# Performance work log

Hardware: AMD Instinct MI355X
Metric: run time of the kernel (lower is better)

## Reference

```python
import jax, jax.numpy as jnp
import numpy as np

H = 4  # fixed number of heads in the layer


def setup_inputs() -> dict:
    key = jax.random.key(0)
    ks = jax.random.split(key, 6)
    B, S, D = 4, 2048, 512
    U = 2 * D  # per-head projection width (units = d_model * 2)
    x = jax.random.normal(ks[0], (B, S, D), dtype=jnp.float32)
    gamma = jnp.ones((D,), dtype=jnp.float32)
    beta = jnp.zeros((D,), dtype=jnp.float32)
    s = 0.02
    Wq = jax.random.normal(ks[1], (H, D, U), dtype=jnp.float32) * s
    Wk = jax.random.normal(ks[2], (H, D, U), dtype=jnp.float32) * s
    Wv = jax.random.normal(ks[3], (H, D, U), dtype=jnp.float32) * s
    Wout = jax.random.normal(ks[4], (H * U, D), dtype=jnp.float32) * s
    return {"x": x, "gamma": gamma, "beta": beta, "Wq": Wq, "Wk": Wk, "Wv": Wv, "Wout": Wout}


def _forward(x, gamma, beta, Wq, Wk, Wv, Wout):
    B, S, D = x.shape
    eps = 1e-6
    # LayerNormalization over last axis (Keras default, eps=1e-6)
    mu = jnp.mean(x, axis=-1, keepdims=True)
    var = jnp.mean(jnp.square(x - mu), axis=-1, keepdims=True)
    xn = (x - mu) * jax.lax.rsqrt(var + eps) * gamma + beta
    # Per-head Q/K/V projections, batched over head axis. Dropout is identity at inference.
    q = jnp.einsum('bsd,hdu->bhsu', xn, Wq)
    k = jnp.einsum('bsd,hdu->bhsu', xn, Wk)
    v = jnp.einsum('bsd,hdu->bhsu', xn, Wv)
    # Keras Attention(use_scale=False, causal=True): unscaled dot-product scores
    scores = jnp.einsum('bhsu,bhtu->bhst', q, k)  # [B,H,S,S]
    causal = jnp.tril(jnp.ones((S, S), dtype=bool))
    scores = jnp.where(causal, scores, jnp.finfo(scores.dtype).min)
    probs = jax.nn.softmax(scores, axis=-1)
    head = jnp.einsum('bhst,bhtu->bhsu', probs, v)  # [B,H,S,U]
    # concat heads in head order -> [B,S,H*U], then output Dense back to D
    HU = head.shape[1] * head.shape[3]
    cat = head.transpose(0, 2, 1, 3).reshape(B, S, HU)
    return cat @ Wout


def reference(x, gamma, beta, Wq, Wk, Wv, Wout):
    return _forward(x, gamma, beta, Wq, Wk, Wv, Wout)
```

## Files before the change

kernel.cpp:

```cpp
#include <hip/hip_runtime.h>

typedef _Float16 half8 __attribute__((ext_vector_type(8)));
typedef float floatx4 __attribute__((ext_vector_type(4)));

__device__ __forceinline__ void gl16(const _Float16* g, _Float16* l) {
    __builtin_amdgcn_global_load_lds((const __attribute__((address_space(1))) void*)g,
                                     (__attribute__((address_space(3))) void*)l, 16, 0, 0);
}

__device__ __forceinline__ half8 dsr16(const _Float16* p) {
    half8 r;
    const __attribute__((address_space(3))) _Float16* lp =
        (const __attribute__((address_space(3))) _Float16*)p;
    asm volatile("ds_read_b128 %0, %1" : "=v"(r) : "v"(lp));
    return r;
}

#define Scst 2048
#define Dcst 512
#define Ucst 1024
#define Hcst 4
#define SDo 1048576LL
#define UDo 524288LL
#define SUo 2097152LL
#define SSo 4194304LL
#define USo 2097152LL
#define SHUo 8388608LL

__global__ __launch_bounds__(64) void ln_k(const float* __restrict__ x,
                                           const float* __restrict__ gamma,
                                           const float* __restrict__ beta,
                                           _Float16* __restrict__ xn) {
    const int D = 512;
    long long base = (long long)blockIdx.x * D;
    int lane = threadIdx.x;
    floatx4 x0 = *(const floatx4*)(x + base + lane * 8);
    floatx4 x1 = *(const floatx4*)(x + base + lane * 8 + 4);
    float f[8];
#pragma unroll
    for (int i = 0; i < 4; i++) { f[i] = x0[i]; f[4 + i] = x1[i]; }
    float s = 0.f, ss = 0.f;
#pragma unroll
    for (int i = 0; i < 8; i++) { s += f[i]; ss += f[i] * f[i]; }
#pragma unroll
    for (int off = 32; off; off >>= 1) { s += __shfl_xor(s, off); ss += __shfl_xor(ss, off); }
    float mean = s * (1.f / 512.f);
    float var = ss * (1.f / 512.f) - mean * mean;
    float rstd = rsqrtf(var + 1e-6f);
    floatx4 g0 = *(const floatx4*)(gamma + lane * 8);
    floatx4 g1 = *(const floatx4*)(gamma + lane * 8 + 4);
    floatx4 b0 = *(const floatx4*)(beta + lane * 8);
    floatx4 b1 = *(const floatx4*)(beta + lane * 8 + 4);
    half8 o;
#pragma unroll
    for (int i = 0; i < 4; i++) {
        o[i]     = (_Float16)((f[i]     - mean) * rstd * g0[i] + b0[i]);
        o[4 + i] = (_Float16)((f[4 + i] - mean) * rstd * g1[i] + b1[i]);
    }
    *(half8*)(xn + base + lane * 8) = o;
}

__global__ __launch_bounds__(256) void tr_k(const float* __restrict__ in,
                                            _Float16* __restrict__ out, int R, int C) {
    __shared__ _Float16 tile[32][33];
    int tx = threadIdx.x, ty = threadIdx.y;
    long long zo = (long long)blockIdx.z * R * C;
    int r0 = blockIdx.y * 32, c0 = blockIdx.x * 32;
    for (int yy = ty; yy < 32; yy += 8)
        tile[yy][tx] = (_Float16)in[zo + (long long)(r0 + yy) * C + c0 + tx];
    __syncthreads();
    for (int yy = ty; yy < 32; yy += 8)
        out[zo + (long long)(c0 + yy) * R + r0 + tx] = tile[tx][yy];
}

#define BM 128
#define BN 128
#define BK 32
__global__ __launch_bounds__(256) void gemm_bt(
    const _Float16* __restrict__ A, const _Float16* __restrict__ Bt, void* __restrict__ Cv,
    int K, int ldc, int cflags, int mode) {
    int z = blockIdx.z;
    long long offA = 0, offB = 0, offC = 0;
    switch (mode) {
        case 1:
            offA = (long long)((z >> 2) & 1) * SDo;
            offB = (long long)(((z >> 3) * 4) + (z & 3)) * UDo;
            offC = (long long)(((z >> 3) * 8) + ((z & 3) * 2) + ((z >> 2) & 1)) * SUo;
            break;
        case 2:
            offA = (long long)z * SUo; offB = (long long)z * SUo; offC = (long long)z * SSo;
            break;
        case 3:
            offA = (long long)(z >> 1) * UDo; offB = (long long)(z & 1) * SDo;
            offC = (long long)z * USo;
            break;
        case 4:
            offA = (long long)z * SSo; offB = (long long)z * USo;
            offC = (long long)(z & 1) * SHUo + (long long)(z >> 1) * Ucst;
            break;
        case 6:
            offB = (long long)(z & 7) * UDo; offC = (long long)z * SUo;
            break;
        case 7:
            offA = (long long)(z & 3) * UDo; offC = (long long)z * USo;
            break;
        default: break;
    }
    const _Float16* Ab = A + offA;
    const _Float16* Bb = Bt + offB;

    int gx = gridDim.x, gy = gridDim.y;
    int nb = gx * gy;
    int lin = blockIdx.y * gx + blockIdx.x;
    int mIdx, nIdx;
    if (((nb & 7) == 0) && ((gx & 3) == 0)) {
        int chunk = nb >> 3;
        int vid = (lin >> 3) + chunk * (lin & 7);
        int panelH = gy * 4;
        int panel = vid / panelH;
        int rem = vid - panel * panelH;
        mIdx = rem >> 2;
        nIdx = (panel << 2) + (rem & 3);
    } else { mIdx = blockIdx.y; nIdx = blockIdx.x; }
    int m0 = mIdx * BM, n0 = nIdx * BN;

    if ((cflags & 4) && n0 > m0 + (BM - 1)) return;
    int kend = (cflags & 8) ? min(K, m0 + BM) : K;

    __shared__ _Float16 As[2][BM * BK];
    __shared__ _Float16 Bs[2][BN * BK];

    int t = threadIdx.x;
    int srow = t >> 2;
    int scol = (t & 3) * 8;
    int lane = t & 63, w = t >> 6;
    int wm = (w >> 1) * 64, wn = (w & 1) * 64;
    int lm = lane & 15, lk = (lane >> 4) * 8;

    floatx4 acc[4][4];
#pragma unroll
    for (int i = 0; i < 4; i++)
#pragma unroll
        for (int j = 0; j < 4; j++) acc[i][j] = floatx4{0.f, 0.f, 0.f, 0.f};

    const _Float16* ga0 = Ab + (long long)(m0 + srow) * K + scol;
    const _Float16* ga1 = Ab + (long long)(m0 + 64 + srow) * K + scol;
    const _Float16* gb0 = Bb + (long long)(n0 + srow) * K + scol;
    const _Float16* gb1 = Bb + (long long)(n0 + 64 + srow) * K + scol;

    int nIter = kend / BK;
    gl16(ga0, &As[0][t * 8]);
    gl16(ga1, &As[0][2048 + t * 8]);
    gl16(gb0, &Bs[0][t * 8]);
    gl16(gb1, &Bs[0][2048 + t * 8]);

    for (int it = 0; it < nIter; it++) {
        __syncthreads();
        int cur = it & 1;
        half8 af[4], bfr[4];
#pragma unroll
        for (int i = 0; i < 4; i++) af[i] = *(const half8*)&As[cur][(wm + i * 16 + lm) * BK + lk];
#pragma unroll
        for (int j = 0; j < 4; j++) bfr[j] = *(const half8*)&Bs[cur][(wn + j * 16 + lm) * BK + lk];
        if (it + 1 < nIter) {
            int nk = (it + 1) * BK;
            int nxt = cur ^ 1;
            gl16(ga0 + nk, &As[nxt][t * 8]);
            gl16(ga1 + nk, &As[nxt][2048 + t * 8]);
            gl16(gb0 + nk, &Bs[nxt][t * 8]);
            gl16(gb1 + nk, &Bs[nxt][2048 + t * 8]);
        }
#pragma unroll
        for (int i = 0; i < 4; i++)
#pragma unroll
            for (int j = 0; j < 4; j++)
                acc[i][j] = __builtin_amdgcn_mfma_f32_16x16x32_f16(af[i], bfr[j], acc[i][j], 0, 0, 0);
    }

    int cr = (lane >> 4) * 4;
    int cc = lm;
    bool outf32 = (cflags & 1) != 0;
#pragma unroll
    for (int i = 0; i < 4; i++) {
#pragma unroll
        for (int j = 0; j < 4; j++) {
            int rr = m0 + wm + i * 16 + cr;
            int nn = n0 + wn + j * 16 + cc;
#pragma unroll
            for (int r2 = 0; r2 < 4; r2++) {
                long long idx = (long long)(rr + r2) * ldc + nn + offC;
                float val = acc[i][j][r2];
                if (outf32) ((float*)Cv)[idx] = val;
                else ((_Float16*)Cv)[idx] = (_Float16)val;
            }
        }
    }
}

__global__ __launch_bounds__(512, 2) void gemm_bt256(
    const _Float16* __restrict__ A, const _Float16* __restrict__ Bt, void* __restrict__ Cv,
    int K, int ldc, int cflags, int mode) {
    int z = blockIdx.z;
    long long offA = 0, offB = 0, offC = 0;
    switch (mode) {
        case 1:
            offA = (long long)((z >> 2) & 1) * SDo;
            offB = (long long)(((z >> 3) * 4) + (z & 3)) * UDo;
            offC = (long long)(((z >> 3) * 8) + ((z & 3) * 2) + ((z >> 2) & 1)) * SUo;
            break;
        case 2:
            offA = (long long)z * SUo; offB = (long long)z * SUo; offC = (long long)z * SSo;
            break;
        case 3:
            offA = (long long)(z >> 1) * UDo; offB = (long long)(z & 1) * SDo;
            offC = (long long)z * USo;
            break;
        case 4:
            offA = (long long)z * SSo; offB = (long long)z * USo;
            offC = (long long)(z & 1) * SHUo + (long long)(z >> 1) * Ucst;
            break;
        default: break;
    }
    const _Float16* Ab = A + offA;
    const _Float16* Bb = Bt + offB;

    int gx = gridDim.x;
    int nwg = gx * gridDim.y;
    int lin = blockIdx.y * gx + blockIdx.x;
    int q8 = nwg >> 3, r8 = nwg & 7;
    int xcd = lin & 7, sub8 = lin >> 3;
    int wg = (xcd < r8 ? xcd * (q8 + 1) : r8 * (q8 + 1) + (xcd - r8) * q8) + sub8;
    int m0 = (wg / gx) * 256, n0 = (wg % gx) * 256;

    if ((cflags & 4) && n0 > m0 + 255) return;
    int kend = (cflags & 8) ? min(K, m0 + 256) : K;
    int NT = kend >> 6;

    __shared__ _Float16 As2[2][2][8192];
    __shared__ _Float16 Bs2[2][2][8192];

    int t = threadIdx.x;
    int lane = t & 63, w = t >> 6;
    int wm = (w >> 2) * 128, wn = (w & 3) * 64;
    int lm = lane & 15, ls = lane >> 4;
    int sw8 = ((ls ^ ((lm >> 1) & 3)) << 3);

    long long stoff = (long long)(t >> 2) * K + (((t & 3) ^ ((t >> 3) & 3)) << 3);
    const _Float16* gA = Ab + (long long)m0 * K + stoff;
    const _Float16* gB = Bb + (long long)n0 * K + stoff;
    long long rowK = 128LL * K;
    int ldd = t * 8;

    floatx4 acc[8][4];
#pragma unroll
    for (int i = 0; i < 8; i++)
#pragma unroll
        for (int j = 0; j < 4; j++) acc[i][j] = floatx4{0.f, 0.f, 0.f, 0.f};

#define STGA(v, ks) { const _Float16* s_ = gA + (((v) << 6) + ((ks) << 5)); \
        gl16(s_, &As2[(v) & 1][ks][ldd]); gl16(s_ + rowK, &As2[(v) & 1][ks][4096 + ldd]); }
#define STGB(v, ks) { const _Float16* s_ = gB + (((v) << 6) + ((ks) << 5)); \
        gl16(s_, &Bs2[(v) & 1][ks][ldd]); gl16(s_ + rowK, &Bs2[(v) & 1][ks][4096 + ldd]); }
#define RDA(mm, ks) dsr16(&As2[cur][ks][(wm + (mm) * 16 + lm) * 32 + sw8])
#define RDB(nn, ks) dsr16(&Bs2[cur][ks][(wn + (nn) * 16 + lm) * 32 + sw8])
#define MFMA16(mh) \
    _Pragma("unroll") for (int mm = 0; mm < 4; mm++) \
    _Pragma("unroll") for (int nn = 0; nn < 4; nn++) \
        acc[(mh) * 4 + mm][nn] = __builtin_amdgcn_mfma_f32_16x16x32_f16( \
            af[mm], bf[nn], acc[(mh) * 4 + mm][nn], 0, 0, 0);

    STGA(0, 0) STGB(0, 0) STGA(0, 1) STGB(0, 1)
    if (NT > 1) { STGA(1, 0) STGB(1, 0) }
    if (NT > 1) asm volatile("s_waitcnt vmcnt(8)" ::: "memory");
    else        asm volatile("s_waitcnt vmcnt(4)" ::: "memory");
    __builtin_amdgcn_s_barrier();

    for (int tt = 0; tt < NT; tt++) {
        int cur = tt & 1;
        half8 af[4], bf[4];
        bf[0] = RDB(0, 0); bf[1] = RDB(1, 0); bf[2] = RDB(2, 0); bf[3] = RDB(3, 0);
        af[0] = RDA(0, 0); af[1] = RDA(1, 0); af[2] = RDA(2, 0); af[3] = RDA(3, 0);
        if (tt + 1 < NT) STGA(tt + 1, 1)
        __builtin_amdgcn_s_barrier();
        asm volatile("s_waitcnt lgkmcnt(0)" ::: "memory");
        __builtin_amdgcn_sched_barrier(0);
        __builtin_amdgcn_s_setprio(1);
        MFMA16(0)
        __builtin_amdgcn_s_setprio(0);
        __builtin_amdgcn_s_barrier();
        af[0] = RDA(4, 0); af[1] = RDA(5, 0); af[2] = RDA(6, 0); af[3] = RDA(7, 0);
        if (tt + 1 < NT) STGB(tt + 1, 1)
        if (tt + 1 < NT) asm volatile("s_waitcnt vmcnt(8)" ::: "memory");
        else             asm volatile("s_waitcnt vmcnt(0)" ::: "memory");
        __builtin_amdgcn_s_barrier();
        asm volatile("s_waitcnt lgkmcnt(0)" ::: "memory");
        __builtin_amdgcn_sched_barrier(0);
        __builtin_amdgcn_s_setprio(1);
        MFMA16(1)
        __builtin_amdgcn_s_setprio(0);
        __builtin_amdgcn_s_barrier();
        bf[0] = RDB(0, 1); bf[1] = RDB(1, 1); bf[2] = RDB(2, 1); bf[3] = RDB(3, 1);
        af[0] = RDA(0, 1); af[1] = RDA(1, 1); af[2] = RDA(2, 1); af[3] = RDA(3, 1);
        if (tt + 2 < NT) STGA(tt + 2, 0)
        __builtin_amdgcn_s_barrier();
        asm volatile("s_waitcnt lgkmcnt(0)" ::: "memory");
        __builtin_amdgcn_sched_barrier(0);
        __builtin_amdgcn_s_setprio(1);
        MFMA16(0)
        __builtin_amdgcn_s_setprio(0);
        __builtin_amdgcn_s_barrier();
        af[0] = RDA(4, 1); af[1] = RDA(5, 1); af[2] = RDA(6, 1); af[3] = RDA(7, 1);
        if (tt + 2 < NT) STGB(tt + 2, 0)
        if (tt + 2 < NT)      asm volatile("s_waitcnt vmcnt(8)" ::: "memory");
        else if (tt + 1 < NT) asm volatile("s_waitcnt vmcnt(4)" ::: "memory");
        else                  asm volatile("s_waitcnt vmcnt(0)" ::: "memory");
        __builtin_amdgcn_s_barrier();
        asm volatile("s_waitcnt lgkmcnt(0)" ::: "memory");
        __builtin_amdgcn_sched_barrier(0);
        __builtin_amdgcn_s_setprio(1);
        MFMA16(1)
        __builtin_amdgcn_s_setprio(0);
        __builtin_amdgcn_s_barrier();
    }

    int cr = ls * 4, cc = lm;
    bool outf32 = (cflags & 1) != 0;
#pragma unroll
    for (int i = 0; i < 8; i++) {
#pragma unroll
        for (int j = 0; j < 4; j++) {
            int rr = m0 + wm + i * 16 + cr;
            int nn = n0 + wn + j * 16 + cc;
#pragma unroll
            for (int r2 = 0; r2 < 4; r2++) {
                long long idx = (long long)(rr + r2) * ldc + nn + offC;
                float val = acc[i][j][r2];
                if (outf32) ((float*)Cv)[idx] = val;
                else ((_Float16*)Cv)[idx] = (_Float16)val;
            }
        }
    }
#undef STGA
#undef STGB
#undef RDA
#undef RDB
#undef MFMA16
}

__global__ __launch_bounds__(256) void softmax_h(_Float16* __restrict__ sc, int S) {
    int wid = threadIdx.x >> 6, lane = threadIdx.x & 63;
    int idx = blockIdx.x * 4 + wid;
    int r = idx & (S - 1);
    _Float16* srow = sc + (long long)idx * S;
    int nc = r >> 9;
    float v[32];
    float mx = -3.0e38f;
    for (int c = 0; c <= nc; c++) {
        half8 hv = *(half8*)(srow + lane * 8 + c * 512);
#pragma unroll
        for (int i = 0; i < 8; i++) {
            int n = lane * 8 + c * 512 + i;
            float s = (n <= r) ? (float)hv[i] : -3.0e38f;
            v[c * 8 + i] = s; mx = fmaxf(mx, s);
        }
    }
#pragma unroll
    for (int off = 32; off; off >>= 1) mx = fmaxf(mx, __shfl_xor(mx, off));
    float sum = 0.f;
    for (int c = 0; c <= nc; c++)
#pragma unroll
        for (int i = 0; i < 8; i++) {
            int n = lane * 8 + c * 512 + i;
            float e = (n <= r) ? __expf(v[c * 8 + i] - mx) : 0.f;
            v[c * 8 + i] = e; sum += e;
        }
#pragma unroll
    for (int off = 32; off; off >>= 1) sum += __shfl_xor(sum, off);
    float inv = 1.f / sum;
    for (int c = 0; c <= nc; c++) {
        half8 o;
#pragma unroll
        for (int i = 0; i < 8; i++) o[i] = (_Float16)(v[c * 8 + i] * inv);
        *(half8*)(srow + lane * 8 + c * 512) = o;
    }
}

extern "C" void kernel_launch(void* const* d_in, const int* in_sizes, int n_in,
                              void* d_out, int out_size, void* d_ws, size_t ws_size,
                              hipStream_t stream) {
    const int B = 4, S = 2048, D = 512, H = 4, U = 1024;
    const float* x     = (const float*)d_in[0];
    const float* gamma = (const float*)d_in[1];
    const float* beta  = (const float*)d_in[2];
    const float* Wq    = (const float*)d_in[3];
    const float* Wk    = (const float*)d_in[4];
    const float* Wv    = (const float*)d_in[5];
    const float* Wout  = (const float*)d_in[6];
    float* out = (float*)d_out;

    char* ws = (char*)d_ws;
    const size_t MiB = 1ull << 20;
    const long long SD = SDo, UD = UDo, SU = SUo, US = USo;

    _Float16* xn  = (_Float16*)(ws + 0);
    _Float16* WqT = (_Float16*)(ws + 8  * MiB);
    _Float16* WkT = (_Float16*)(ws + 12 * MiB);
    _Float16* WvT = (_Float16*)(ws + 16 * MiB);
    _Float16* WoT = (_Float16*)(ws + 20 * MiB);

    tr_k<<<dim3(U / 32, D / 32, H), dim3(32, 8), 0, stream>>>(Wq, WqT, D, U);
    tr_k<<<dim3(U / 32, D / 32, H), dim3(32, 8), 0, stream>>>(Wk, WkT, D, U);
    tr_k<<<dim3(U / 32, D / 32, H), dim3(32, 8), 0, stream>>>(Wv, WvT, D, U);
    tr_k<<<dim3(D / 32, (H * U) / 32, 1), dim3(32, 8), 0, stream>>>(Wout, WoT, H * U, D);
    ln_k<<<B * S, 64, 0, stream>>>(x, gamma, beta, xn);

    if (ws_size >= 168 * MiB) {
        _Float16* qk  = (_Float16*)(ws + 24 * MiB);
        _Float16* kk  = qk + 8 * SU;
        _Float16* sc  = (_Float16*)(ws + 88 * MiB);
        _Float16* vt  = qk;
        _Float16* cat = kk;

        for (int p = 0; p < 2; p++) {
            const _Float16* xnp = xn + (long long)p * 2 * SD;
            float* outp = out + (long long)p * 2 * SD;
            gemm_bt256<<<dim3(U / 256, S / 256, 16), 512, 0, stream>>>(xnp, WqT, qk, D, U, 0, 1);
            gemm_bt256<<<dim3(S / 256, S / 256, 8), 512, 0, stream>>>(qk, kk, sc, U, S, 4, 2);
            softmax_h<<<8 * S / 4, 256, 0, stream>>>(sc, S);
            gemm_bt256<<<dim3(S / 256, U / 256, 8), 512, 0, stream>>>(WvT, xnp, vt, D, S, 0, 3);
            gemm_bt256<<<dim3(U / 256, S / 256, 8), 512, 0, stream>>>(sc, vt, cat, S, H * U, 8, 4);
            gemm_bt<<<dim3(D / 128, 2 * S / 128, 1), 256, 0, stream>>>(cat, WoT, outp,
                H * U, D, 1, 0);
        }
    } else {
        _Float16* qb   = (_Float16*)(ws + 24 * MiB);
        _Float16* vTb  = (_Float16*)(ws + 56 * MiB);
        _Float16* catb = (_Float16*)(ws + 72 * MiB);
        _Float16* sc   = (_Float16*)(ws + 88 * MiB);

        for (int b = 0; b < B; b++) {
            const _Float16* xnb = xn + (long long)b * SD;
            gemm_bt<<<dim3(U / 128, S / 128, 2 * H), 256, 0, stream>>>(xnb, WqT, qb, D, U, 0, 6);
            gemm_bt<<<dim3(S / 128, U / 128, H), 256, 0, stream>>>(WvT, xnb, vTb, D, S, 0, 7);
            for (int h = 0; h < H; h++) {
                gemm_bt<<<dim3(S / 128, S / 128, 1), 256, 0, stream>>>(qb + (long long)h * SU,
                    qb + (long long)(H + h) * SU, sc, U, S, 4, 0);
                softmax_h<<<S / 4, 256, 0, stream>>>(sc, S);
                gemm_bt<<<dim3(U / 128, S / 128, 1), 256, 0, stream>>>(sc,
                    vTb + (long long)h * US, (void*)(catb + (long long)h * U), S, H * U, 8, 0);
            }
            gemm_bt<<<dim3(D / 128, S / 128, 1), 256, 0, stream>>>(catb, WoT,
                (void*)(out + (long long)b * SD), H * U, D, 1, 0);
        }
    }
}
```

Before: 663.5 us.

## Restructure GEMM main loop to two barriers per K-step with staggered LDS waits

The GEMM main loop is rebuilt so each K-substep loads all eight A fragments and four B fragments at once, with one barrier per substep instead of four. Partial lgkmcnt waits let the first half of the MFMAs start while the remaining LDS reads are still in flight. The global-to-LDS prefetches for A and B are now issued together after each MFMA block. This removes barrier stalls but raises register pressure (eight A fragments live). It also drops the NT==1 guard in the prologue, which assumes at least two K tiles.

```diff
diff --git a/kernel.cpp b/kernel.cpp
--- a/kernel.cpp
+++ b/kernel.cpp
@@ -263,64 +263,50 @@
         gl16(s_, &Bs2[(v) & 1][ks][ldd]); gl16(s_ + rowK, &Bs2[(v) & 1][ks][4096 + ldd]); }
 #define RDA(mm, ks) dsr16(&As2[cur][ks][(wm + (mm) * 16 + lm) * 32 + sw8])
 #define RDB(nn, ks) dsr16(&Bs2[cur][ks][(wn + (nn) * 16 + lm) * 32 + sw8])
-#define MFMA16(mh) \
-    _Pragma("unroll") for (int mm = 0; mm < 4; mm++) \
+#define MFMAH(m0_, m1_) \
+    _Pragma("unroll") for (int mm = (m0_); mm < (m1_); mm++) \
     _Pragma("unroll") for (int nn = 0; nn < 4; nn++) \
-        acc[(mh) * 4 + mm][nn] = __builtin_amdgcn_mfma_f32_16x16x32_f16( \
-            af[mm], bf[nn], acc[(mh) * 4 + mm][nn], 0, 0, 0);
-
-    STGA(0, 0) STGB(0, 0) STGA(0, 1) STGB(0, 1)
-    if (NT > 1) { STGA(1, 0) STGB(1, 0) }
-    if (NT > 1) asm volatile("s_waitcnt vmcnt(8)" ::: "memory");
-    else        asm volatile("s_waitcnt vmcnt(4)" ::: "memory");
+        acc[mm][nn] = __builtin_amdgcn_mfma_f32_16x16x32_f16( \
+            af[mm], bf[nn], acc[mm][nn], 0, 0, 0);
+
+    STGA(0, 0) STGB(0, 0) STGA(0, 1) STGB(0, 1) STGA(1, 0) STGB(1, 0)
+    asm volatile("s_waitcnt vmcnt(8)" ::: "memory");
     __builtin_amdgcn_s_barrier();
 
     for (int tt = 0; tt < NT; tt++) {
         int cur = tt & 1;
-        half8 af[4], bf[4];
+        half8 af[8], bf[4];
+        bool more = (tt + 1 < NT);
         bf[0] = RDB(0, 0); bf[1] = RDB(1, 0); bf[2] = RDB(2, 0); bf[3] = RDB(3, 0);
         af[0] = RDA(0, 0); af[1] = RDA(1, 0); af[2] = RDA(2, 0); af[3] = RDA(3, 0);
-        if (tt + 1 < NT) STGA(tt + 1, 1)
+        af[4] = RDA(4, 0); af[5] = RDA(5, 0); af[6] = RDA(6, 0); af[7] = RDA(7, 0);
+        if (more) asm volatile("s_waitcnt vmcnt(4)" ::: "memory");
+        else      asm volatile("s_waitcnt vmcnt(0)" ::: "memory");
         __builtin_amdgcn_s_barrier();
+        asm volatile("s_waitcnt lgkmcnt(4)" ::: "memory");
+        __builtin_amdgcn_sched_barrier(0);
+        __builtin_amdgcn_s_setprio(1);
+        MFMAH(0, 4)
         asm volatile("s_waitcnt lgkmcnt(0)" ::: "memory");
         __builtin_amdgcn_sched_barrier(0);
+        MFMAH(4, 8)
+        __builtin_amdgcn_s_setprio(0);
+        if (more) { STGA(tt + 1, 1) STGB(tt + 1, 1) }
+        bf[0] = RDB(0, 1); bf[1] = RDB(1, 1); bf[2] = RDB(2, 1); bf[3] = RDB(3, 1);
+        af[0] = RDA(0, 1); af[1] = RDA(1, 1); af[2] = RDA(2, 1); af[3] = RDA(3, 1);
+        af[4] = RDA(4, 1); af[5] = RDA(5, 1); af[6] = RDA(6, 1); af[7] = RDA(7, 1);
+        if (more) asm volatile("s_waitcnt vmcnt(4)" ::: "memory");
+        else      asm volatile("s_waitcnt vmcnt(0)" ::: "memory");
+        __builtin_amdgcn_s_barrier();
+        asm volatile("s_waitcnt lgkmcnt(4)" ::: "memory");
+        __builtin_amdgcn_sched_barrier(0);
         __builtin_amdgcn_s_setprio(1);
-        MFMA16(0)
-        __builtin_amdgcn_s_setprio(0);
-        __builtin_amdgcn_s_barrier();
-        af[0] = RDA(4, 0); af[1] = RDA(5, 0); af[2] = RDA(6, 0); af[3] = RDA(7, 0);
-        if (tt + 1 < NT) STGB(tt + 1, 1)
-        if (tt + 1 < NT) asm volatile("s_waitcnt vmcnt(8)" ::: "memory");
-        else             asm volatile("s_waitcnt vmcnt(0)" ::: "memory");
-        __builtin_amdgcn_s_barrier();
+        MFMAH(0, 4)
         asm volatile("s_waitcnt lgkmcnt(0)" ::: "memory");
         __builtin_amdgcn_sched_barrier(0);
-        __builtin_amdgcn_s_setprio(1);
-        MFMA16(1)
+        MFMAH(4, 8)
         __builtin_amdgcn_s_setprio(0);
-        __builtin_amdgcn_s_barrier();
-        bf[0] = RDB(0, 1); bf[1] = RDB(1, 1); bf[2] = RDB(2, 1); bf[3] = RDB(3, 1);
-        af[0] = RDA(0, 1); af[1] = RDA(1, 1); af[2] = RDA(2, 1); af[3] = RDA(3, 1);
-        if (tt + 2 < NT) STGA(tt + 2, 0)
-        __builtin_amdgcn_s_barrier();
-        asm volatile("s_waitcnt lgkmcnt(0)" ::: "memory");
-        __builtin_amdgcn_sched_barrier(0);
-        __builtin_amdgcn_s_setprio(1);
-        MFMA16(0)
-        __builtin_amdgcn_s_setprio(0);
-        __builtin_amdgcn_s_barrier();
-        af[0] = RDA(4, 1); af[1] = RDA(5, 1); af[2] = RDA(6, 1); af[3] = RDA(7, 1);
-        if (tt + 2 < NT) STGB(tt + 2, 0)
-        if (tt + 2 < NT)      asm volatile("s_waitcnt vmcnt(8)" ::: "memory");
-        else if (tt + 1 < NT) asm volatile("s_waitcnt vmcnt(4)" ::: "memory");
-        else                  asm volatile("s_waitcnt vmcnt(0)" ::: "memory");
-        __builtin_amdgcn_s_barrier();
-        asm volatile("s_waitcnt lgkmcnt(0)" ::: "memory");
-        __builtin_amdgcn_sched_barrier(0);
-        __builtin_amdgcn_s_setprio(1);
-        MFMA16(1)
-        __builtin_amdgcn_s_setprio(0);
-        __builtin_amdgcn_s_barrier();
+        if (tt + 2 < NT) { STGA(tt + 2, 0) STGB(tt + 2, 0) }
     }
 
     int cr = ls * 4, cc = lm;
@@ -344,7 +330,7 @@
 #undef STGB
 #undef RDA
 #undef RDB
-#undef MFMA16
+#undef MFMAH
 }
 
 __global__ __launch_bounds__(256) void softmax_h(_Float16* __restrict__ sc, int S) {
```

Result: slower. 696.5 us (+5.0%).
